# Optimization experiments

Measured on AMD Instinct MI355X. Metric: run time of the kernel, lower is better.

## Reference

```python
import jax, jax.numpy as jnp
import numpy as np
import math

B, S, H, N = 1, 4096, 1024, 16
HN = H // N  # 64

def setup_inputs() -> dict:
    key = jax.random.key(0)
    k1, k2, k3 = jax.random.split(key, 3)
    hidden_states = jax.random.normal(k1, (B, S, H), dtype=jnp.float32)
    # lower-triangular causal mask, float {0,1}, broadcastable to [b,np,s,s]
    ltor_mask = jnp.tril(jnp.ones((1, 1, S, S), dtype=jnp.float32))
    w_qkv = jax.random.normal(k2, (3 * H, H), dtype=jnp.float32) * 0.02
    b_qkv = jnp.zeros((3 * H,), dtype=jnp.float32)
    w_dense = jax.random.normal(k3, (H, H), dtype=jnp.float32) * 0.02
    b_dense = jnp.zeros((H,), dtype=jnp.float32)
    return {"hidden_states": hidden_states, "ltor_mask": ltor_mask,
            "w_qkv": w_qkv, "b_qkv": b_qkv,
            "w_dense": w_dense, "b_dense": b_dense}

def reference(hidden_states, ltor_mask, w_qkv, b_qkv, w_dense, b_dense):
    b, s, h = hidden_states.shape
    # fused QKV projection: [b,s,3h]
    mixed = jnp.einsum('bsh,oh->bso', hidden_states, w_qkv) + b_qkv
    q, k, v = jnp.split(mixed, 3, axis=-1)
    # [b,s,h] -> [b,n,s,hn]
    def heads(t):
        return t.reshape(b, s, N, HN).transpose(0, 2, 1, 3)
    q, k, v = heads(q), heads(k), heads(v)
    # raw scores [b,n,s,s]
    scores = jnp.einsum('bnqd,bnkd->bnqk', q, k) / math.sqrt(HN)
    # multiplicative mask plus -10000 additive for masked positions
    scores = scores * ltor_mask - 10000.0 * (1.0 - ltor_mask)
    probs = jax.nn.softmax(scores, axis=-1)
    # attention dropout prob = 0.0 -> identity
    ctx = jnp.einsum('bnqk,bnkd->bnqd', probs, v)
    ctx = ctx.transpose(0, 2, 1, 3).reshape(b, s, h)
    out = jnp.einsum('bsh,oh->bso', ctx, w_dense) + b_dense
    # output dropout prob = 0.0 -> identity
    return out
```

## Files before the change

kernel.cpp:

```cpp
#include <hip/hip_runtime.h>
#include <hip/hip_bf16.h>

static constexpr int SEQ  = 4096;
static constexpr int HID  = 1024;
static constexpr int NHEAD = 16;
static constexpr int HDIM  = 64;
static constexpr int H3   = 3072;

typedef __attribute__((ext_vector_type(8))) __bf16 bf16x8;
typedef __attribute__((ext_vector_type(4))) float  f32x4;

__device__ __forceinline__ float bf2f(unsigned short u) {
    union { unsigned int u; float f; } v; v.u = ((unsigned int)u) << 16; return v.f;
}
__device__ __forceinline__ unsigned short f2bf(float f) {
    union { float f; unsigned int u; } v; v.f = f;
    unsigned int r = v.u + 0x7fffu + ((v.u >> 16) & 1u);
    return (unsigned short)(r >> 16);
}
__device__ __forceinline__ void gl_lds16(const unsigned short* g, unsigned short* l) {
    __builtin_amdgcn_global_load_lds(
        (const __attribute__((address_space(1))) void*)g,
        (__attribute__((address_space(3))) void*)l, 16, 0, 0);
}

struct Conv5 { const float* src[5]; unsigned short* dst[5]; };

__global__ __launch_bounds__(256) void convert5(Conv5 c) {
    constexpr int cnt[5]  = {4194304, 3145728, 3072, 1048576, 1024};
    constexpr int boff[5] = {0, 2048, 3584, 3586, 4098};
    const int b = blockIdx.x;
    int t = 0, rel = b;
#pragma unroll
    for (int k = 1; k < 5; ++k) if (b >= boff[k]) { t = k; rel = b - boff[k]; }
    const int base = rel * 2048 + threadIdx.x * 8;
    if (base >= cnt[t]) return;
    const float* s = c.src[t] + base;
    const float4 a = ((const float4*)s)[0];
    const float4 b2 = ((const float4*)s)[1];
    union { unsigned short v[8]; uint4 q; } u;
    u.v[0] = f2bf(a.x); u.v[1] = f2bf(a.y); u.v[2] = f2bf(a.z); u.v[3] = f2bf(a.w);
    u.v[4] = f2bf(b2.x); u.v[5] = f2bf(b2.y); u.v[6] = f2bf(b2.z); u.v[7] = f2bf(b2.w);
    *(uint4*)(c.dst[t] + base) = u.q;
}

template <int BM, int BN, int BK, typename OutT, bool VFUSE>
__global__ __launch_bounds__(256) void gemm_bt(
    const unsigned short* __restrict__ A, const unsigned short* __restrict__ B,
    const unsigned short* __restrict__ bias, OutT* __restrict__ C,
    unsigned short* __restrict__ vt,
    int M, int N, int K)
{
    constexpr int MI  = BM / 32;
    constexpr int NI  = BN / 32;
    constexpr int KC  = BK / 32;
    constexpr int CB  = BK / 8;
    constexpr int LSH = (BK == 32) ? 2 : ((BK == 64) ? 3 : 4);
    constexpr int RPC = 64 >> LSH;

    const int tid  = threadIdx.x;
    const int wave = tid >> 6, lane = tid & 63;
    const int quad = lane >> 4, c16 = lane & 15;

    constexpr int GM = 8;
    const int nxB = N / BN, nyB = M / BM;
    const int per_group = GM * nxB;
    const int gid = blockIdx.x / per_group;
    const int rem = blockIdx.x % per_group;
    const int gm  = (nyB - gid * GM < GM) ? (nyB - gid * GM) : GM;
    const int by  = gid * GM + rem % gm;
    const int bxn = rem / gm;
    const int m0 = by * BM, n0 = bxn * BN;
    const int wr = wave >> 1, wc = wave & 1;

    __shared__ __align__(16) unsigned short sA[BM * BK];
    __shared__ __align__(16) unsigned short sB[BN * BK];

    f32x4 acc[MI][NI];
#pragma unroll
    for (int i = 0; i < MI; ++i)
#pragma unroll
        for (int j = 0; j < NI; ++j) acc[i][j] = {0.f, 0.f, 0.f, 0.f};

    const int sr = lane >> LSH;
    const int sl = lane & (CB - 1);

    for (int k0 = 0; k0 < K; k0 += BK) {
#pragma unroll
        for (int cc = 0; cc < BM / RPC / 4; ++cc) {
            const int rbase = cc * (4 * RPC) + wave * RPC;
            const int row = rbase + sr;
            const int sc = (sl ^ (row & (CB - 1))) * 8;
            gl_lds16(A + (size_t)(m0 + row) * K + k0 + sc, &sA[rbase * BK]);
        }
#pragma unroll
        for (int cc = 0; cc < BN / RPC / 4; ++cc) {
            const int rbase = cc * (4 * RPC) + wave * RPC;
            const int row = rbase + sr;
            const int sc = (sl ^ (row & (CB - 1))) * 8;
            gl_lds16(B + (size_t)(n0 + row) * K + k0 + sc, &sB[rbase * BK]);
        }
        __syncthreads();

#pragma unroll
        for (int kc = 0; kc < KC; ++kc) {
            bf16x8 af[MI], bfr[NI];
#pragma unroll
            for (int i = 0; i < MI; ++i) {
                const int ra = wr * (BM / 2) + i * 16 + c16;
                af[i] = *(const bf16x8*)&sA[ra * BK + (((kc * 4 + quad) ^ ra) & (CB - 1)) * 8];
            }
#pragma unroll
            for (int j = 0; j < NI; ++j) {
                const int rb = wc * (BN / 2) + j * 16 + c16;
                bfr[j] = *(const bf16x8*)&sB[rb * BK + (((kc * 4 + quad) ^ rb) & (CB - 1)) * 8];
            }
#pragma unroll
            for (int i = 0; i < MI; ++i)
#pragma unroll
                for (int j = 0; j < NI; ++j)
                    acc[i][j] = __builtin_amdgcn_mfma_f32_16x16x32_bf16(af[i], bfr[j], acc[i][j], 0, 0, 0);
        }
        __syncthreads();
    }

    if constexpr (VFUSE) {
        if (n0 >= 2048) {
#pragma unroll
            for (int j = 0; j < NI; ++j) {
                const int col = n0 + wc * (BN / 2) + j * 16 + c16;
                const float bv = bf2f(bias[col]);
                const int d  = col - 2048;
                unsigned short* vrow = vt + (size_t)d * SEQ;
#pragma unroll
                for (int i = 0; i < MI; ++i) {
                    const int base32 = m0 + wr * (BM / 2) + (i >> 1) * 32;
                    const int phys = base32 + 8 * quad + 4 * (i & 1);
                    union { unsigned short u[4]; uint2 q2; } w;
#pragma unroll
                    for (int r = 0; r < 4; ++r) w.u[r] = f2bf(acc[i][j][r] + bv);
                    *(uint2*)&vrow[phys] = w.q2;
                }
            }
            return;
        }
    }

#pragma unroll
    for (int j = 0; j < NI; ++j) {
        const int col = n0 + wc * (BN / 2) + j * 16 + c16;
        const float bv = bf2f(bias[col]);
#pragma unroll
        for (int i = 0; i < MI; ++i) {
#pragma unroll
            for (int r = 0; r < 4; ++r) {
                const int row = m0 + wr * (BM / 2) + i * 16 + quad * 4 + r;
                const float v = acc[i][j][r] + bv;
                if constexpr (sizeof(OutT) == 2) C[(size_t)row * N + col] = (OutT)f2bf(v);
                else                             C[(size_t)row * N + col] = (OutT)v;
            }
        }
    }
}

__global__ __launch_bounds__(256) void attn_causal(
    const unsigned short* __restrict__ qkv, const unsigned short* __restrict__ vt,
    unsigned short* __restrict__ ctx)
{
    const int bx = blockIdx.x;
    const int n  = bx & 15;
    const int z0 = bx >> 4;
    const int z  = (z0 < 32) ? z0 : 95 - z0;
    const int tid  = threadIdx.x;
    const int wave = tid >> 6, lane = tid & 63;
    const int quad = lane >> 4, c16 = lane & 15;
    const int qg  = wave & 1;
    const int kvh = wave >> 1;

    __shared__ __align__(16) unsigned short smem[16384];
    unsigned short* smem_k = smem;
    unsigned short* smem_v = smem + 8192;

    const int qrow0 = z * 64 + qg * 32;

    const float QS = 0.125f * 1.44269504f;
    bf16x8 qf[2][2];
#pragma unroll
    for (int wq = 0; wq < 2; ++wq)
#pragma unroll
        for (int kc = 0; kc < 2; ++kc) {
            bf16x8 q = *(const bf16x8*)(qkv + (size_t)(qrow0 + wq * 16 + c16) * H3 + n * HDIM + kc * 32 + quad * 8);
#pragma unroll
            for (int j = 0; j < 8; ++j) q[j] = (__bf16)((float)q[j] * QS);
            qf[wq][kc] = q;
        }

    f32x4 o[2][4];
#pragma unroll
    for (int wq = 0; wq < 2; ++wq)
#pragma unroll
        for (int dt = 0; dt < 4; ++dt) o[wq][dt] = {0.f, 0.f, 0.f, 0.f};
    float l_i[2] = {0.f, 0.f};

    const int srow8 = lane >> 3;
    const int scol8 = ((lane & 7) ^ (lane >> 3)) * 8;
    const int srow4 = lane >> 4;

    const int nkb = (z + 2) >> 1;
    for (int kb = 0; kb < nkb; ++kb) {
        const int kv0 = kb * 128;
#pragma unroll
        for (int cc = 0; cc < 4; ++cc) {
            const int rb = wave * 32 + cc * 8;
            gl_lds16(qkv + (size_t)(kv0 + rb + srow8) * H3 + HID + n * HDIM + scol8,
                     &smem_k[rb * 64]);
        }
#pragma unroll
        for (int cc = 0; cc < 4; ++cc) {
            const int rb = wave * 16 + cc * 4;
            const int sv = (((lane & 15) ^ ((cc * 4 + srow4) & 15))) * 8;
            gl_lds16(vt + (size_t)(n * HDIM + rb + srow4) * SEQ + kv0 + sv,
                     &smem_v[rb * 128]);
        }
        __syncthreads();

        const int kv0w = kv0 + kvh * 64;
        if (kv0w <= qrow0 + 31) {
            f32x4 s[2][4];
#pragma unroll
            for (int wq = 0; wq < 2; ++wq)
#pragma unroll
                for (int mt = 0; mt < 4; ++mt) s[wq][mt] = {0.f, 0.f, 0.f, 0.f};
#pragma unroll
            for (int mt = 0; mt < 4; ++mt) {
                const int krow = kvh * 64 + mt * 16 + c16;
                const bf16x8 kf0 = *(const bf16x8*)&smem_k[krow * 64 + ((quad)     ^ (krow & 7)) * 8];
                const bf16x8 kf1 = *(const bf16x8*)&smem_k[krow * 64 + ((4 + quad) ^ (krow & 7)) * 8];
#pragma unroll
                for (int wq = 0; wq < 2; ++wq) {
                    s[wq][mt] = __builtin_amdgcn_mfma_f32_16x16x32_bf16(kf0, qf[wq][0], s[wq][mt], 0, 0, 0);
                    s[wq][mt] = __builtin_amdgcn_mfma_f32_16x16x32_bf16(kf1, qf[wq][1], s[wq][mt], 0, 0, 0);
                }
            }

#pragma unroll
            for (int wq = 0; wq < 2; ++wq) {
                if (kv0w + 63 > qrow0 + wq * 16) {
                    const int q_g = qrow0 + wq * 16 + c16;
#pragma unroll
                    for (int mt = 0; mt < 4; ++mt)
#pragma unroll
                        for (int r = 0; r < 4; ++r) {
                            const int kv = kv0w + mt * 16 + quad * 4 + r;
                            if (kv > q_g) s[wq][mt][r] = -30000.0f;
                        }
                }
                float rs = 0.f;
#pragma unroll
                for (int mt = 0; mt < 4; ++mt)
#pragma unroll
                    for (int r = 0; r < 4; ++r) {
                        const float p = __builtin_amdgcn_exp2f(s[wq][mt][r]);
                        s[wq][mt][r] = p;
                        rs += p;
                    }
                l_i[wq] += rs;
            }

            bf16x8 pf[2][2];
#pragma unroll
            for (int wq = 0; wq < 2; ++wq)
#pragma unroll
                for (int kc = 0; kc < 2; ++kc) {
                    union { __bf16 b[8]; bf16x8 v; } pp;
#pragma unroll
                    for (int r = 0; r < 4; ++r) {
                        pp.b[r]     = (__bf16)s[wq][2 * kc][r];
                        pp.b[4 + r] = (__bf16)s[wq][2 * kc + 1][r];
                    }
                    pf[wq][kc] = pp.v;
                }

#pragma unroll
            for (int kc = 0; kc < 2; ++kc) {
#pragma unroll
                for (int dt = 0; dt < 4; ++dt) {
                    const int vrow = dt * 16 + c16;
                    const int pc8 = (kvh * 8 + kc * 4 + quad) ^ (vrow & 15);
                    const bf16x8 vf = *(const bf16x8*)&smem_v[vrow * 128 + pc8 * 8];
#pragma unroll
                    for (int wq = 0; wq < 2; ++wq)
                        o[wq][dt] = __builtin_amdgcn_mfma_f32_16x16x32_bf16(vf, pf[wq][kc], o[wq][dt], 0, 0, 0);
                }
            }
        }
        __syncthreads();
    }

#pragma unroll
    for (int wq = 0; wq < 2; ++wq) {
        l_i[wq] += __shfl_xor(l_i[wq], 16);
        l_i[wq] += __shfl_xor(l_i[wq], 32);
    }

    float* cb = (float*)smem;
    float* lb = (float*)(smem + 8704);
    unsigned short* fb = smem + 8832;

    if (kvh == 0) {
#pragma unroll
        for (int wq = 0; wq < 2; ++wq) {
#pragma unroll
            for (int dt = 0; dt < 4; ++dt)
                *(f32x4*)&cb[(qg * 32 + wq * 16 + c16) * 68 + dt * 16 + quad * 4] = o[wq][dt];
            if (quad == 0) lb[qg * 32 + wq * 16 + c16] = l_i[wq];
        }
    }
    __syncthreads();
    if (kvh == 1) {
#pragma unroll
        for (int wq = 0; wq < 2; ++wq) {
            const float inv = 1.0f / (l_i[wq] + lb[qg * 32 + wq * 16 + c16]);
#pragma unroll
            for (int dt = 0; dt < 4; ++dt) {
                const f32x4 p = *(const f32x4*)&cb[(qg * 32 + wq * 16 + c16) * 68 + dt * 16 + quad * 4];
                union { unsigned short u[4]; uint2 q2; } w;
#pragma unroll
                for (int r = 0; r < 4; ++r) w.u[r] = f2bf((o[wq][dt][r] + p[r]) * inv);
                *(uint2*)&fb[(qg * 32 + wq * 16 + c16) * 72 + dt * 16 + quad * 4] = w.q2;
            }
        }
    }
    __syncthreads();

    const int qr = tid >> 2;
    const int xc = (tid & 3) * 16;
    unsigned short* dst = ctx + (size_t)(z * 64 + qr) * HID + n * HDIM + xc;
    *(uint4*)dst       = *(const uint4*)&fb[qr * 72 + xc];
    *(uint4*)(dst + 8) = *(const uint4*)&fb[qr * 72 + xc + 8];
}

extern "C" void kernel_launch(void* const* d_in, const int* in_sizes, int n_in,
                              void* d_out, int out_size, void* d_ws, size_t ws_size,
                              hipStream_t stream)
{
    unsigned short* base = (unsigned short*)d_ws;

    unsigned short* hs_c = base;
    unsigned short* wq_c = hs_c + 4194304;
    unsigned short* bq_c = wq_c + 3145728;
    unsigned short* wd_c = bq_c + 3072;
    unsigned short* bd_c = wd_c + 1048576;
    unsigned short* qkv  = bd_c + 1024;
    unsigned short* vt   = qkv + (size_t)SEQ * H3;
    unsigned short* ctx  = hs_c;

    Conv5 c;
    c.src[0] = (const float*)d_in[0]; c.src[1] = (const float*)d_in[2];
    c.src[2] = (const float*)d_in[3]; c.src[3] = (const float*)d_in[4];
    c.src[4] = (const float*)d_in[5];
    c.dst[0] = hs_c; c.dst[1] = wq_c; c.dst[2] = bq_c; c.dst[3] = wd_c; c.dst[4] = bd_c;
    hipLaunchKernelGGL(convert5, dim3(4099), dim3(256), 0, stream, c);

    hipLaunchKernelGGL((gemm_bt<128, 128, 64, unsigned short, true>),
                       dim3((H3 / 128) * (SEQ / 128)), dim3(256), 0, stream,
                       hs_c, wq_c, bq_c, qkv, vt, SEQ, H3, HID);

    hipLaunchKernelGGL(attn_causal, dim3(NHEAD * (SEQ / 64)), dim3(256), 0, stream,
                       qkv, vt, ctx);

    hipLaunchKernelGGL((gemm_bt<64, 128, 128, float, false>),
                       dim3((HID / 128) * (SEQ / 64)), dim3(256), 0, stream,
                       ctx, wd_c, bd_c, (float*)d_out, (unsigned short*)nullptr, SEQ, HID, HID);
}
```

Measured before the change: 236.8 us.

## Compute softmax row sums via MFMA with ones and split attention into two launches

The per-element scalar accumulation of exponentials is replaced by an extra MFMA that multiplies a ones vector by the bf16 probability fragments. This removes the VALU adds and the cross-lane shuffle reduction, but the denominator is now summed from bf16-rounded probabilities, which matches the numerator. Separately, the attention grid is split into two launches by even/odd query-block parity, with each half pairing light and heavy causal blocks. This adds one kernel launch and a serialization point between the halves.

```diff
diff --git a/kernel.cpp b/kernel.cpp
--- a/kernel.cpp
+++ b/kernel.cpp
@@ -165,11 +165,11 @@
 
 __global__ __launch_bounds__(256) void attn_causal(
     const unsigned short* __restrict__ qkv, const unsigned short* __restrict__ vt,
-    unsigned short* __restrict__ ctx)
+    unsigned short* __restrict__ ctx, int dpar)
 {
     const int bx = blockIdx.x;
     const int n  = bx & 15;
-    const int z0 = bx >> 4;
+    const int z0 = ((bx >> 4) << 1) | dpar;
     const int z  = (z0 < 32) ? z0 : 95 - z0;
     const int tid  = threadIdx.x;
     const int wave = tid >> 6, lane = tid & 63;
@@ -195,12 +195,16 @@
             qf[wq][kc] = q;
         }
 
+    bf16x8 onesf;
+#pragma unroll
+    for (int j = 0; j < 8; ++j) onesf[j] = (__bf16)1.0f;
+
     f32x4 o[2][4];
 #pragma unroll
     for (int wq = 0; wq < 2; ++wq)
 #pragma unroll
         for (int dt = 0; dt < 4; ++dt) o[wq][dt] = {0.f, 0.f, 0.f, 0.f};
-    float l_i[2] = {0.f, 0.f};
+    f32x4 lacc[2] = {{0.f, 0.f, 0.f, 0.f}, {0.f, 0.f, 0.f, 0.f}};
 
     const int srow8 = lane >> 3;
     const int scol8 = ((lane & 7) ^ (lane >> 3)) * 8;
@@ -255,16 +259,11 @@
                             if (kv > q_g) s[wq][mt][r] = -30000.0f;
                         }
                 }
-                float rs = 0.f;
 #pragma unroll
                 for (int mt = 0; mt < 4; ++mt)
 #pragma unroll
-                    for (int r = 0; r < 4; ++r) {
-                        const float p = __builtin_amdgcn_exp2f(s[wq][mt][r]);
-                        s[wq][mt][r] = p;
-                        rs += p;
-                    }
-                l_i[wq] += rs;
+                    for (int r = 0; r < 4; ++r)
+                        s[wq][mt][r] = __builtin_amdgcn_exp2f(s[wq][mt][r]);
             }
 
             bf16x8 pf[2][2];
@@ -282,6 +281,12 @@
                 }
 
 #pragma unroll
+            for (int wq = 0; wq < 2; ++wq)
+#pragma unroll
+                for (int kc = 0; kc < 2; ++kc)
+                    lacc[wq] = __builtin_amdgcn_mfma_f32_16x16x32_bf16(onesf, pf[wq][kc], lacc[wq], 0, 0, 0);
+
+#pragma unroll
             for (int kc = 0; kc < 2; ++kc) {
 #pragma unroll
                 for (int dt = 0; dt < 4; ++dt) {
@@ -297,11 +302,7 @@
         __syncthreads();
     }
 
-#pragma unroll
-    for (int wq = 0; wq < 2; ++wq) {
-        l_i[wq] += __shfl_xor(l_i[wq], 16);
-        l_i[wq] += __shfl_xor(l_i[wq], 32);
-    }
+    const float l_i[2] = { lacc[0][0], lacc[1][0] };
 
     float* cb = (float*)smem;
     float* lb = (float*)(smem + 8704);
@@ -366,8 +367,10 @@
                        dim3((H3 / 128) * (SEQ / 128)), dim3(256), 0, stream,
                        hs_c, wq_c, bq_c, qkv, vt, SEQ, H3, HID);
 
-    hipLaunchKernelGGL(attn_causal, dim3(NHEAD * (SEQ / 64)), dim3(256), 0, stream,
-                       qkv, vt, ctx);
+    hipLaunchKernelGGL(attn_causal, dim3(512), dim3(256), 0, stream,
+                       qkv, vt, ctx, 0);
+    hipLaunchKernelGGL(attn_causal, dim3(512), dim3(256), 0, stream,
+                       qkv, vt, ctx, 1);
 
     hipLaunchKernelGGL((gemm_bt<64, 128, 128, float, false>),
                        dim3((HID / 128) * (SEQ / 64)), dim3(256), 0, stream,
```

Result: slower. 269.3 us (+13.7%).

## Fuse output dense projection into attention kernel via per-row-block completion counters

Applied to the files above, without the earlier changes.

Removes the separate output GEMM launch. Each attention block bumps an atomic counter for its 64-row query block once its context tile is written. Half of the blocks (heads 0-7) then spin until all 16 heads are done and compute a 64x128 slice of the dense projection from the context rows. This saves a kernel launch and lets the projection overlap with attention tail work. The cost is spin-waiting blocks that hold CUs, a risk of deadlock if waiting blocks are resident before the producers they wait on, and a less tuned GEMM tile with no double buffering.

```diff
diff --git a/kernel.cpp b/kernel.cpp
--- a/kernel.cpp
+++ b/kernel.cpp
@@ -165,7 +165,9 @@
 
 __global__ __launch_bounds__(256) void attn_causal(
     const unsigned short* __restrict__ qkv, const unsigned short* __restrict__ vt,
-    unsigned short* __restrict__ ctx)
+    unsigned short* __restrict__ ctx,
+    const unsigned short* __restrict__ wd, const unsigned short* __restrict__ bd,
+    float* __restrict__ out, unsigned int* __restrict__ done)
 {
     const int bx = blockIdx.x;
     const int n  = bx & 15;
@@ -338,6 +340,85 @@
     unsigned short* dst = ctx + (size_t)(z * 64 + qr) * HID + n * HDIM + xc;
     *(uint4*)dst       = *(const uint4*)&fb[qr * 72 + xc];
     *(uint4*)(dst + 8) = *(const uint4*)&fb[qr * 72 + xc + 8];
+
+    __syncthreads();
+    if (tid == 0) {
+        __threadfence();
+        atomicAdd(&done[z], 1u);
+    }
+
+    if (n >= 8) return;
+    if (tid == 0) {
+        while (atomicAdd(&done[z], 0u) < 16u) __builtin_amdgcn_s_sleep(8);
+        __threadfence();
+    }
+    __syncthreads();
+
+    unsigned short* s2A = smem;
+    unsigned short* s2B = smem + 4096;
+    const int wr2 = wave >> 1, wc2 = wave & 1;
+    const int sr8 = lane >> 3;
+    const int sl8 = lane & 7;
+    const int m0 = z * 64, n0 = n * 128;
+
+    f32x4 acc2[2][4];
+#pragma unroll
+    for (int i = 0; i < 2; ++i)
+#pragma unroll
+        for (int j = 0; j < 4; ++j) acc2[i][j] = {0.f, 0.f, 0.f, 0.f};
+
+    for (int k0 = 0; k0 < HID; k0 += 64) {
+#pragma unroll
+        for (int cc = 0; cc < 2; ++cc) {
+            const int rbase = cc * 32 + wave * 8;
+            const int row = rbase + sr8;
+            const int sc = (sl8 ^ (row & 7)) * 8;
+            gl_lds16(ctx + (size_t)(m0 + row) * HID + k0 + sc, &s2A[rbase * 64]);
+        }
+#pragma unroll
+        for (int cc = 0; cc < 4; ++cc) {
+            const int rbase = cc * 32 + wave * 8;
+            const int row = rbase + sr8;
+            const int sc = (sl8 ^ (row & 7)) * 8;
+            gl_lds16(wd + (size_t)(n0 + row) * HID + k0 + sc, &s2B[rbase * 64]);
+        }
+        __syncthreads();
+
+#pragma unroll
+        for (int kc = 0; kc < 2; ++kc) {
+            bf16x8 af[2], bfr[4];
+#pragma unroll
+            for (int i = 0; i < 2; ++i) {
+                const int ra = wr2 * 32 + i * 16 + c16;
+                af[i] = *(const bf16x8*)&s2A[ra * 64 + (((kc * 4 + quad) ^ ra) & 7) * 8];
+            }
+#pragma unroll
+            for (int j = 0; j < 4; ++j) {
+                const int rb = wc2 * 64 + j * 16 + c16;
+                bfr[j] = *(const bf16x8*)&s2B[rb * 64 + (((kc * 4 + quad) ^ rb) & 7) * 8];
+            }
+#pragma unroll
+            for (int i = 0; i < 2; ++i)
+#pragma unroll
+                for (int j = 0; j < 4; ++j)
+                    acc2[i][j] = __builtin_amdgcn_mfma_f32_16x16x32_bf16(af[i], bfr[j], acc2[i][j], 0, 0, 0);
+        }
+        __syncthreads();
+    }
+
+#pragma unroll
+    for (int j = 0; j < 4; ++j) {
+        const int col = n0 + wc2 * 64 + j * 16 + c16;
+        const float bv = bf2f(bd[col]);
+#pragma unroll
+        for (int i = 0; i < 2; ++i) {
+#pragma unroll
+            for (int r = 0; r < 4; ++r) {
+                const int row = m0 + wr2 * 32 + i * 16 + quad * 4 + r;
+                out[(size_t)row * HID + col] = acc2[i][j][r] + bv;
+            }
+        }
+    }
 }
 
 extern "C" void kernel_launch(void* const* d_in, const int* in_sizes, int n_in,
@@ -354,6 +435,9 @@
     unsigned short* qkv  = bd_c + 1024;
     unsigned short* vt   = qkv + (size_t)SEQ * H3;
     unsigned short* ctx  = hs_c;
+    unsigned int*  done  = (unsigned int*)(vt + 4194304);
+
+    hipMemsetAsync(done, 0, 64 * sizeof(unsigned int), stream);
 
     Conv5 c;
     c.src[0] = (const float*)d_in[0]; c.src[1] = (const float*)d_in[2];
@@ -367,9 +451,5 @@
                        hs_c, wq_c, bq_c, qkv, vt, SEQ, H3, HID);
 
     hipLaunchKernelGGL(attn_causal, dim3(NHEAD * (SEQ / 64)), dim3(256), 0, stream,
-                       qkv, vt, ctx);
-
-    hipLaunchKernelGGL((gemm_bt<64, 128, 128, float, false>),
-                       dim3((HID / 128) * (SEQ / 64)), dim3(256), 0, stream,
-                       ctx, wd_c, bd_c, (float*)d_out, (unsigned short*)nullptr, SEQ, HID, HID);
-}
+                       qkv, vt, ctx, wd_c, bd_c, (float*)d_out, done);
+}
```

Result: slower. 312.5 us (+32.0%).
